# Optimization experiments

Hardware: AMD Instinct MI355X
Metric: run time of the kernel (lower is better)

Reference implementation:

```python
import jax, jax.numpy as jnp
import numpy as np
import math

B, S, HID = 2, 2048, 2048
H, HKV, D, L = 16, 4, 128, 64
THETA = 10000.0
N_REP = H // HKV


def _rope(t, pos, theta=THETA):
    # t: [B, h, S, D], pos: [B, S] int
    d = t.shape[-1]
    inv_freq = 1.0 / (theta ** (jnp.arange(0, d, 2, dtype=jnp.float32) / d))  # [d/2]
    ang = pos.astype(jnp.float32)[:, :, None] * inv_freq  # [B, S, d/2]
    cos = jnp.concatenate([jnp.cos(ang), jnp.cos(ang)], axis=-1)[:, None]  # [B,1,S,d]
    sin = jnp.concatenate([jnp.sin(ang), jnp.sin(ang)], axis=-1)[:, None]
    t1, t2 = t[..., : d // 2], t[..., d // 2 :]
    rot = jnp.concatenate([-t2, t1], axis=-1)
    return t * cos + rot * sin


def setup_inputs() -> dict:
    key = jax.random.key(0)
    ks = jax.random.split(key, 9)
    sc = lambda fin: 1.0 / math.sqrt(fin)
    x = jax.random.normal(ks[0], (B, S, HID), dtype=jnp.float32)
    position_ids = jnp.broadcast_to(jnp.arange(S, dtype=jnp.int32), (B, S))
    # additive causal mask [1,1,S,S]
    causal = jnp.triu(jnp.full((S, S), -1e9, dtype=jnp.float32), k=1)
    attention_mask = causal[None, None]
    Wq = jax.random.normal(ks[1], (HID, H * D), dtype=jnp.float32) * sc(HID)
    Wk = jax.random.normal(ks[2], (HID, HKV * D), dtype=jnp.float32) * sc(HID)
    Wv = jax.random.normal(ks[3], (HID, HKV * D), dtype=jnp.float32) * sc(HID)
    Wql = jax.random.normal(ks[4], (D, L), dtype=jnp.float32) * sc(D)
    Wkl = jax.random.normal(ks[5], (D, L), dtype=jnp.float32) * sc(D)
    Wvl = jax.random.normal(ks[6], (D, L), dtype=jnp.float32) * sc(D)
    Wo = jax.random.normal(ks[7], (H * D, HID), dtype=jnp.float32) * sc(H * D)
    return {"x": x, "position_ids": position_ids, "attention_mask": attention_mask,
            "Wq": Wq, "Wk": Wk, "Wv": Wv, "Wql": Wql, "Wkl": Wkl, "Wvl": Wvl, "Wo": Wo}


def reference(x, position_ids, attention_mask, Wq, Wk, Wv, Wql, Wkl, Wvl, Wo):
    b, s, _ = x.shape
    q = (x @ Wq).reshape(b, s, H, D).transpose(0, 2, 1, 3)    # [B,H,S,D]
    k = (x @ Wk).reshape(b, s, HKV, D).transpose(0, 2, 1, 3)  # [B,HKV,S,D]
    v = (x @ Wv).reshape(b, s, HKV, D).transpose(0, 2, 1, 3)
    q = _rope(q, position_ids)
    k = _rope(k, position_ids)
    # latent compression per head-dim
    q_l = jnp.einsum('bhsd,dl->bhsl', q, Wql)  # [B,H,S,L]
    k_l = jnp.einsum('bhsd,dl->bhsl', k, Wkl)  # [B,HKV,S,L]
    v_l = jnp.einsum('bhsd,dl->bhsl', v, Wvl)
    k_l = jnp.repeat(k_l, N_REP, axis=1)  # repeat_kv -> [B,H,S,L]
    v_l = jnp.repeat(v_l, N_REP, axis=1)
    scale = math.sqrt(L)
    attn = jnp.einsum('bhql,bhkl->bhqk', q_l, k_l) / scale
    attn = attn + attention_mask
    attn = jax.nn.softmax(attn, axis=-1)
    out = jnp.einsum('bhqk,bhkl->bhql', attn, v_l)  # [B,H,S,L]
    if L < D:
        out = jnp.pad(out, ((0, 0), (0, 0), (0, 0), (0, D - L)))
    out = out.transpose(0, 2, 1, 3).reshape(b, s, H * D)
    return out @ Wo
```

## Files before the change

### kernel.cpp

```cpp
#include <hip/hip_runtime.h>
#include <cstddef>

constexpr int kB   = 2;
constexpr int kS   = 2048;
constexpr int kHID = 2048;
constexpr int kH   = 16;
constexpr int kHKV = 4;
constexpr int kD   = 128;
constexpr int kL   = 64;
constexpr int kTok = kB * kS;
constexpr int kNQKV = kH * kD + 2 * kHKV * kD;

typedef __attribute__((ext_vector_type(8))) short bf16x8;
typedef __attribute__((ext_vector_type(4))) float f32x4;

static __device__ __forceinline__ short f2bf(float f) {
  union { float f; unsigned u; } v{f};
  const unsigned r = (v.u + 0x7fff + ((v.u >> 16) & 1)) >> 16;
  return (short)r;
}
static __device__ __forceinline__ float bf2f(short s) {
  union { unsigned u; float f; } v;
  v.u = ((unsigned)(unsigned short)s) << 16;
  return v.f;
}

static __device__ __forceinline__ bf16x8 pack8(float4 a, float4 b) {
  bf16x8 r;
  r[0] = f2bf(a.x); r[1] = f2bf(a.y); r[2] = f2bf(a.z); r[3] = f2bf(a.w);
  r[4] = f2bf(b.x); r[5] = f2bf(b.y); r[6] = f2bf(b.z); r[7] = f2bf(b.w);
  return r;
}

static __device__ __forceinline__ unsigned cvt_pk_bf16(float lo, float hi) {
  unsigned r;
  asm("v_cvt_pk_bf16_f32 %0, %1, %2" : "=v"(r) : "v"(lo), "v"(hi));
  return r;
}

typedef __attribute__((address_space(3))) void       lds_void;
typedef __attribute__((address_space(1))) const void gm_void;
static __device__ __forceinline__ void gload16(const void* g, void* l) {
  __builtin_amdgcn_global_load_lds((gm_void*)g, (lds_void*)l, 16, 0, 0);
}

static __device__ __forceinline__ int2 xcd_swz(int nx, int ny) {
  int wg = blockIdx.y * nx + blockIdx.x;
  const int cpx = (nx * ny) >> 3;
  wg = (wg & 7) * cpx + (wg >> 3);
  int2 r; r.x = wg % nx; r.y = wg / nx;
  return r;
}

__global__ __launch_bounds__(256) void cvt_bf16(const float* __restrict__ in,
                                                short* __restrict__ out, int n8) {
  const int i = blockIdx.x * 256 + threadIdx.x;
  if (i >= n8) return;
  const float4 a = *(const float4*)&in[i * 8];
  const float4 b = *(const float4*)&in[i * 8 + 4];
  *(bf16x8*)&out[i * 8] = pack8(a, b);
}

__global__ __launch_bounds__(256) void trig_table(const int* __restrict__ pos,
                                                  float* __restrict__ tbl) {
  const int idx = blockIdx.x * 256 + threadIdx.x;
  if (idx >= kTok * 64) return;
  const int i = idx & 63, t = idx >> 6;
  const float p = (float)pos[t];
  const float inv_freq = expf(-(float)i * (9.210340371976184f / 64.0f));
  const float ang = p * inv_freq;
  tbl[t * 128 + i]      = cosf(ang);
  tbl[t * 128 + 64 + i] = sinf(ang);
}

__global__ __launch_bounds__(256) void transpose_qkv(
    const float* __restrict__ Wq, const float* __restrict__ Wk,
    const float* __restrict__ Wv, short* __restrict__ out) {
  __shared__ float T[64][65];
  const int n0 = blockIdx.x * 64, k0 = blockIdx.y * 64;
  const float* in; int Nin, nl0;
  if (n0 < 2048)      { in = Wq; Nin = 2048; nl0 = n0; }
  else if (n0 < 2560) { in = Wk; Nin = 512;  nl0 = n0 - 2048; }
  else                { in = Wv; Nin = 512;  nl0 = n0 - 2560; }
  const int tid = threadIdx.x;
  const int rr = tid >> 4, cc = tid & 15;
#pragma unroll
  for (int ii = 0; ii < 4; ++ii) {
    const int kr = rr + ii * 16;
    const float4 v = *(const float4*)&in[(size_t)(k0 + kr) * Nin + nl0 + cc * 4];
    T[kr][cc * 4 + 0] = v.x; T[kr][cc * 4 + 1] = v.y;
    T[kr][cc * 4 + 2] = v.z; T[kr][cc * 4 + 3] = v.w;
  }
  __syncthreads();
#pragma unroll
  for (int ii = 0; ii < 4; ++ii) {
    const int n = rr + ii * 16;
    const short4 s4 = make_short4(f2bf(T[cc * 4 + 0][n]), f2bf(T[cc * 4 + 1][n]),
                                  f2bf(T[cc * 4 + 2][n]), f2bf(T[cc * 4 + 3][n]));
    *(short4*)&out[(size_t)(n0 + n) * kHID + k0 + cc * 4] = s4;
  }
}

template <bool REMAP>
__global__ __launch_bounds__(256) void transpose_cvt(
    const float* __restrict__ in, short* __restrict__ out,
    int Nin, int out_ld, int row_off, float scale) {
  __shared__ float T[64][65];
  const int tid = threadIdx.x;
  const int k0 = blockIdx.y * 64, n0 = blockIdx.x * 64;
  const int rr = tid >> 4;
  const int cc = tid & 15;
#pragma unroll
  for (int ii = 0; ii < 4; ++ii) {
    const int kr = rr + ii * 16;
    int gr = k0 + kr;
    if (REMAP) gr = ((gr >> 6) << 7) + (gr & 63);
    const float4 v = *(const float4*)&in[(size_t)gr * Nin + n0 + cc * 4];
    T[kr][cc * 4 + 0] = v.x * scale; T[kr][cc * 4 + 1] = v.y * scale;
    T[kr][cc * 4 + 2] = v.z * scale; T[kr][cc * 4 + 3] = v.w * scale;
  }
  __syncthreads();
#pragma unroll
  for (int ii = 0; ii < 4; ++ii) {
    const int n = rr + ii * 16;
    const short4 s4 = make_short4(f2bf(T[cc * 4 + 0][n]), f2bf(T[cc * 4 + 1][n]),
                                  f2bf(T[cc * 4 + 2][n]), f2bf(T[cc * 4 + 3][n]));
    *(short4*)&out[(size_t)(row_off + n0 + n) * out_ld + k0 + cc * 4] = s4;
  }
}

__global__ __launch_bounds__(256) void transpose_lat3(
    const float* __restrict__ Wql, const float* __restrict__ Wkl,
    const float* __restrict__ Wvl, short* __restrict__ WqlT,
    short* __restrict__ WklT, short* __restrict__ WvlT) {
  __shared__ float T[64][65];
  const float* in; short* out; float scale;
  if (blockIdx.z == 0)      { in = Wql; out = WqlT; scale = 0.125f; }
  else if (blockIdx.z == 1) { in = Wkl; out = WklT; scale = 1.0f; }
  else                      { in = Wvl; out = WvlT; scale = 1.0f; }
  const int tid = threadIdx.x;
  const int k0 = blockIdx.y * 64;
  const int rr = tid >> 4, cc = tid & 15;
#pragma unroll
  for (int ii = 0; ii < 4; ++ii) {
    const int kr = rr + ii * 16;
    const float4 v = *(const float4*)&in[(size_t)(k0 + kr) * kL + cc * 4];
    T[kr][cc * 4 + 0] = v.x * scale; T[kr][cc * 4 + 1] = v.y * scale;
    T[kr][cc * 4 + 2] = v.z * scale; T[kr][cc * 4 + 3] = v.w * scale;
  }
  __syncthreads();
#pragma unroll
  for (int ii = 0; ii < 4; ++ii) {
    const int n = rr + ii * 16;
    const short4 s4 = make_short4(f2bf(T[cc * 4 + 0][n]), f2bf(T[cc * 4 + 1][n]),
                                  f2bf(T[cc * 4 + 2][n]), f2bf(T[cc * 4 + 3][n]));
    *(short4*)&out[(size_t)n * kD + k0 + cc * 4] = s4;
  }
}

__global__ __launch_bounds__(512) void gemm_qkv8(
    const short* __restrict__ A, const short* __restrict__ Bt,
    short* __restrict__ C0, short* __restrict__ C1, short* __restrict__ C2,
    int K) {
  __shared__ short As[2][256 * 64];
  __shared__ short Bs[2][256 * 64];
  const int tid = threadIdx.x;
  const int lane = tid & 63, w = tid >> 6;
  const int lr = lane & 15, lk = lane >> 4;
  const int wm = w >> 2, wn = w & 3;
  const int2 sw = xcd_swz(kNQKV / 256, kTok / 256);
  const int row0 = sw.y * 256, col0 = sw.x * 256;
  const int NT = K >> 6;

  auto stage = [&](int kt) {
    const int b = kt & 1;
    const int k0 = kt << 6;
#pragma unroll
    for (int j = 0; j < 4; ++j) {
      const int idx = j * 512 + tid;
      const int row = idx >> 3, blk = idx & 7;
      const int gcol = k0 + ((blk ^ (row & 7)) << 3);
      gload16(A + (size_t)(row0 + row) * K + gcol, &As[b][row * 64 + blk * 8]);
    }
#pragma unroll
    for (int j = 0; j < 4; ++j) {
      const int idx = j * 512 + tid;
      const int row = idx >> 3, blk = idx & 7;
      const int gcol = k0 + ((blk ^ (row & 7)) << 3);
      gload16(Bt + (size_t)(col0 + row) * K + gcol, &Bs[b][row * 64 + blk * 8]);
    }
  };

  f32x4 acc[8][4] = {};

  stage(0);
  for (int t = 0; t < NT; ++t) {
    const int b = t & 1;
    if (t + 1 < NT) {
      stage(t + 1);
      asm volatile("s_waitcnt vmcnt(8)" ::: "memory");
    } else {
      asm volatile("s_waitcnt vmcnt(0)" ::: "memory");
    }
    __builtin_amdgcn_s_barrier();

    bf16x8 bb[4][2];
#pragma unroll
    for (int n = 0; n < 4; ++n) {
      const int row = wn * 64 + n * 16 + lr;
#pragma unroll
      for (int ch = 0; ch < 2; ++ch) {
        const int blk = (ch * 4 + lk) ^ (row & 7);
        bb[n][ch] = *(const bf16x8*)&Bs[b][row * 64 + blk * 8];
      }
    }
#pragma unroll
    for (int qm = 0; qm < 2; ++qm) {
      bf16x8 a[4][2];
#pragma unroll
      for (int j = 0; j < 4; ++j) {
        const int row = wm * 128 + (qm * 4 + j) * 16 + lr;
#pragma unroll
        for (int ch = 0; ch < 2; ++ch) {
          const int blk = (ch * 4 + lk) ^ (row & 7);
          a[j][ch] = *(const bf16x8*)&As[b][row * 64 + blk * 8];
        }
      }
      __builtin_amdgcn_s_setprio(1);
#pragma unroll
      for (int j = 0; j < 4; ++j)
#pragma unroll
        for (int n = 0; n < 4; ++n)
#pragma unroll
          for (int ch = 0; ch < 2; ++ch)
            acc[qm * 4 + j][n] = __builtin_amdgcn_mfma_f32_16x16x32_bf16(
                a[j][ch], bb[n][ch], acc[qm * 4 + j][n], 0, 0, 0);
      __builtin_amdgcn_s_setprio(0);
    }
    __builtin_amdgcn_s_barrier();
  }

  short* dst; int ld, cb;
  if (col0 < 2048)      { dst = C0; ld = 2048; cb = col0; }
  else if (col0 < 2560) { dst = C1; ld = 512;  cb = col0 - 2048; }
  else                  { dst = C2; ld = 512;  cb = col0 - 2560; }
  const int crow0 = row0 + wm * 128 + lk * 4;
  const int ccol0 = cb + wn * 64 + lr;
#pragma unroll
  for (int mf = 0; mf < 8; ++mf)
#pragma unroll
    for (int nf = 0; nf < 4; ++nf)
#pragma unroll
      for (int r = 0; r < 4; ++r)
        dst[(size_t)(crow0 + mf * 16 + r) * ld + ccol0 + nf * 16] =
            f2bf(acc[mf][nf][r]);
}

__global__ __launch_bounds__(512) void gemm_out8(
    const short* __restrict__ A, const short* __restrict__ Bt,
    float* __restrict__ C, int M, int N, int K) {
  __shared__ short As[2][256 * 64];
  __shared__ short Bs[2][128 * 64];
  const int tid = threadIdx.x;
  const int lane = tid & 63, w = tid >> 6;
  const int lr = lane & 15, lk = lane >> 4;
  const int wm = w >> 2, wn = w & 3;
  const int2 sw = xcd_swz(N / 128, M / 256);
  const int row0 = sw.y * 256, col0 = sw.x * 128;
  const int NT = K >> 6;

  auto stage = [&](int kt) {
    const int b = kt & 1;
    const int k0 = kt << 6;
#pragma unroll
    for (int j = 0; j < 4; ++j) {
      const int idx = j * 512 + tid;
      const int row = idx >> 3, blk = idx & 7;
      const int gcol = k0 + ((blk ^ (row & 7)) << 3);
      gload16(A + (size_t)(row0 + row) * K + gcol, &As[b][row * 64 + blk * 8]);
    }
#pragma unroll
    for (int j = 0; j < 2; ++j) {
      const int idx = j * 512 + tid;
      const int row = idx >> 3, blk = idx & 7;
      const int gcol = k0 + ((blk ^ (row & 7)) << 3);
      gload16(Bt + (size_t)(col0 + row) * K + gcol, &Bs[b][row * 64 + blk * 8]);
    }
  };

  f32x4 acc[8][2] = {};

  stage(0);
  for (int t = 0; t < NT; ++t) {
    const int b = t & 1;
    if (t + 1 < NT) {
      stage(t + 1);
      asm volatile("s_waitcnt vmcnt(6)" ::: "memory");
    } else {
      asm volatile("s_waitcnt vmcnt(0)" ::: "memory");
    }
    __builtin_amdgcn_s_barrier();

    bf16x8 bb[2][2];
#pragma unroll
    for (int n = 0; n < 2; ++n) {
      const int row = wn * 32 + n * 16 + lr;
#pragma unroll
      for (int ch = 0; ch < 2; ++ch) {
        const int blk = (ch * 4 + lk) ^ (row & 7);
        bb[n][ch] = *(const bf16x8*)&Bs[b][row * 64 + blk * 8];
      }
    }
#pragma unroll
    for (int qm = 0; qm < 2; ++qm) {
      bf16x8 a[4][2];
#pragma unroll
      for (int j = 0; j < 4; ++j) {
        const int row = wm * 128 + (qm * 4 + j) * 16 + lr;
#pragma unroll
        for (int ch = 0; ch < 2; ++ch) {
          const int blk = (ch * 4 + lk) ^ (row & 7);
          a[j][ch] = *(const bf16x8*)&As[b][row * 64 + blk * 8];
        }
      }
      __builtin_amdgcn_s_setprio(1);
#pragma unroll
      for (int j = 0; j < 4; ++j)
#pragma unroll
        for (int n = 0; n < 2; ++n)
#pragma unroll
          for (int ch = 0; ch < 2; ++ch)
            acc[qm * 4 + j][n] = __builtin_amdgcn_mfma_f32_16x16x32_bf16(
                a[j][ch], bb[n][ch], acc[qm * 4 + j][n], 0, 0, 0);
      __builtin_amdgcn_s_setprio(0);
    }
    __builtin_amdgcn_s_barrier();
  }

  const int crow0 = row0 + wm * 128 + lk * 4;
  const int ccol0 = col0 + wn * 32 + lr;
#pragma unroll
  for (int mf = 0; mf < 8; ++mf)
#pragma unroll
    for (int nf = 0; nf < 2; ++nf)
#pragma unroll
      for (int r = 0; r < 4; ++r)
        C[(size_t)(crow0 + mf * 16 + r) * N + ccol0 + nf * 16] = acc[mf][nf][r];
}

__global__ __launch_bounds__(256) void rope_latent_all(
    const short* __restrict__ qb, const short* __restrict__ kb,
    const short* __restrict__ vb, const short* __restrict__ WqlT,
    const short* __restrict__ WklT, const short* __restrict__ WvlT,
    const float* __restrict__ tbl, short* __restrict__ q_l,
    short* __restrict__ k_l, short* __restrict__ v_lT) {
  __shared__ short Tw[4][1280];
  const int yz = blockIdx.y;
  const short* in; const short* WT; short* out; int nh; bool ROPE, TR;
  int bh;
  if (yz < 32)      { in = qb; WT = WqlT; out = q_l;  nh = kH;   ROPE = true;  TR = false; bh = yz; }
  else if (yz < 40) { in = kb; WT = WklT; out = k_l;  nh = kHKV; ROPE = true;  TR = false; bh = yz - 32; }
  else              { in = vb; WT = WvlT; out = v_lT; nh = kHKV; ROPE = false; TR = true;  bh = yz - 40; }

  const int tid = threadIdx.x;
  const int lane = tid & 63;
  const int w = tid >> 6;
  const int lr = lane & 15;
  const int lk = lane >> 4;
  const int b = bh / nh, h = bh % nh;
  const int s0 = blockIdx.x * 64;
  const int srow = s0 + w * 16 + lr;
  const int tok = b * kS + srow;

  const short* ip = in + ((size_t)tok * nh + h) * kD + lk * 8;
  bf16x8 raw[4];
#pragma unroll
  for (int ch = 0; ch < 4; ++ch) raw[ch] = *(const bf16x8*)(ip + ch * 32);

  bf16x8 af[4];
  if (ROPE) {
    float a[4][8];
#pragma unroll
    for (int ch = 0; ch < 4; ++ch)
#pragma unroll
      for (int i = 0; i < 8; ++i) a[ch][i] = bf2f(raw[ch][i]);
    const float* tb = tbl + (size_t)tok * 128;
    float c[2][8], sn[2][8];
#pragma unroll
    for (int g = 0; g < 2; ++g) {
      const float4 cA = *(const float4*)(tb + g * 32 + lk * 8);
      const float4 cB = *(const float4*)(tb + g * 32 + lk * 8 + 4);
      const float4 sA = *(const float4*)(tb + 64 + g * 32 + lk * 8);
      const float4 sB = *(const float4*)(tb + 64 + g * 32 + lk * 8 + 4);
      c[g][0] = cA.x; c[g][1] = cA.y; c[g][2] = cA.z; c[g][3] = cA.w;
      c[g][4] = cB.x; c[g][5] = cB.y; c[g][6] = cB.z; c[g][7] = cB.w;
      sn[g][0] = sA.x; sn[g][1] = sA.y; sn[g][2] = sA.z; sn[g][3] = sA.w;
      sn[g][4] = sB.x; sn[g][5] = sB.y; sn[g][6] = sB.z; sn[g][7] = sB.w;
    }
    float o[4][8];
#pragma unroll
    for (int g = 0; g < 2; ++g)
#pragma unroll
      for (int i = 0; i < 8; ++i) {
        o[g][i]     = a[g][i]     * c[g][i] - a[g + 2][i] * sn[g][i];
        o[g + 2][i] = a[g + 2][i] * c[g][i] + a[g][i]     * sn[g][i];
      }
#pragma unroll
    for (int ch = 0; ch < 4; ++ch)
#pragma unroll
      for (int i = 0; i < 8; ++i) af[ch][i] = f2bf(o[ch][i]);
  } else {
#pragma unroll
    for (int ch = 0; ch < 4; ++ch) af[ch] = raw[ch];
  }

  f32x4 acc[4] = {};
#pragma unroll
  for (int cb = 0; cb < 4; ++cb) {
#pragma unroll
    for (int ch = 0; ch < 4; ++ch) {
      const bf16x8 bfrag =
          *(const bf16x8*)&WT[(size_t)(cb * 16 + lr) * kD + ch * 32 + lk * 8];
      acc[cb] = __builtin_amdgcn_mfma_f32_16x16x32_bf16(af[ch], bfrag,
                                                        acc[cb], 0, 0, 0);
    }
  }

  short* T = Tw[w];
  if (!TR) {
#pragma unroll
    for (int cb = 0; cb < 4; ++cb)
#pragma unroll
      for (int r = 0; r < 4; ++r)
        T[(lk * 4 + r) * 72 + cb * 16 + lr] = f2bf(acc[cb][r]);
    asm volatile("s_waitcnt lgkmcnt(0)" ::: "memory");
#pragma unroll
    for (int it = 0; it < 2; ++it) {
      const int idx = it * 64 + lane;
      const int row = idx >> 3, c8 = (idx & 7) << 3;
      *(bf16x8*)&out[((size_t)bh * kS + s0 + w * 16 + row) * kL + c8] =
          *(const bf16x8*)&T[row * 72 + c8];
    }
  } else {
#pragma unroll
    for (int cb = 0; cb < 4; ++cb)
#pragma unroll
      for (int r = 0; r < 4; ++r)
        T[(cb * 16 + lr) * 20 + lk * 4 + r] = f2bf(acc[cb][r]);
    asm volatile("s_waitcnt lgkmcnt(0)" ::: "memory");
    const size_t orow = ((size_t)bh * kL + lane) * kS + s0 + w * 16;
#pragma unroll
    for (int c = 0; c < 4; ++c)
      *(short4*)&out[orow + c * 4] = *(const short4*)&T[lane * 20 + c * 4];
  }
}

__global__ __launch_bounds__(512) void flash_attn_mfma(
    const short* __restrict__ ql, const short* __restrict__ kl,
    const short* __restrict__ vlT, short* __restrict__ attn_out) {
  constexpr int LDK = 72;
  __shared__ short Kt[2][64 * LDK];
  __shared__ short Vt[2][64 * LDK];

  const int tid = threadIdx.x;
  const int lane = tid & 63;
  const int w = tid >> 6;
  const int lr = lane & 15;
  const int lk = lane >> 4;
  const int bid = blockIdx.y;
  const int bx = (bid < 8) ? (2 * bid) : (31 - 2 * bid);
  const int q0 = bx * 128;
  const int bh = blockIdx.x;
  const int b = bh >> 4, h = bh & 15;
  const int hk = h >> 2;
  const int wrow = q0 + w * 16;

  const short* qrow = ql + ((size_t)bh * kS + wrow + lr) * kL;
  bf16x8 qf[2];
  qf[0] = *(const bf16x8*)(qrow + lk * 8);
  qf[1] = *(const bf16x8*)(qrow + 32 + lk * 8);

  f32x4 Of[4] = {};
  float m = -3.0e38f, l = 0.f;

  const size_t kbase = (size_t)(b * kHKV + hk) * kS * kL;
  const size_t vbase = (size_t)(b * kHKV + hk) * kL * kS;
  const int ntiles = q0 / 64 + 2;
  const int sr = tid >> 3, sc8 = (tid & 7) << 3;
  const short* kp = kl + kbase + (size_t)sr * kL + sc8;
  const short* vp = vlT + vbase + (size_t)sr * kS + sc8;

  *(bf16x8*)&Kt[0][sr * LDK + sc8] = *(const bf16x8*)kp;
  *(bf16x8*)&Vt[0][sr * LDK + sc8] = *(const bf16x8*)vp;
  __syncthreads();

  const int sl0 = lr + ((lane & 16) << 1);
  const bool hi = (lk >> 1) != 0;

  int cur = 0;
  for (int t = 0; t < ntiles; ++t) {
    const int j0 = t * 64;
    const bool pre = (t + 1 < ntiles);
    bf16x8 krn, vrn;
    if (pre) {
      krn = *(const bf16x8*)(kp + (size_t)(j0 + 64) * kL);
      vrn = *(const bf16x8*)(vp + (j0 + 64));
    }

    if (j0 <= wrow) {
      const short* Kc = &Kt[cur][0];
      const short* Vc = &Vt[cur][0];

      f32x4 Sf[4];
      __builtin_amdgcn_s_setprio(1);
#pragma unroll
      for (int cb = 0; cb < 4; ++cb) {
        f32x4 acc = {};
#pragma unroll
        for (int ch = 0; ch < 2; ++ch) {
          const bf16x8 kf = *(const bf16x8*)&Kc[(cb * 16 + lr) * LDK + ch * 32 + lk * 8];
          acc = __builtin_amdgcn_mfma_f32_16x16x32_bf16(kf, qf[ch], acc, 0, 0, 0);
        }
        Sf[cb] = acc;
      }
      __builtin_amdgcn_s_setprio(0);

      float mt = -3.0e38f;
      if (j0 + 63 > wrow) {
#pragma unroll
        for (int cb = 0; cb < 4; ++cb)
#pragma unroll
          for (int r = 0; r < 4; ++r) {
            float s = Sf[cb][r];
            if ((j0 + cb * 16 + lk * 4 + r) > (wrow + lr)) s = -3.0e38f;
            Sf[cb][r] = s;
            mt = fmaxf(mt, s);
          }
      } else {
#pragma unroll
        for (int cb = 0; cb < 4; ++cb)
#pragma unroll
          for (int r = 0; r < 4; ++r) mt = fmaxf(mt, Sf[cb][r]);
      }
      mt = fmaxf(mt, __shfl_xor(mt, 16));
      mt = fmaxf(mt, __shfl_xor(mt, 32));

      const bool resc = __any((int)(mt > m + 8.f));
      if (resc) {
        const float mnew = fmaxf(m, mt);
        const float corr = __expf(m - mnew);
        m = mnew;
        l *= corr;
#pragma unroll
        for (int lb = 0; lb < 4; ++lb)
#pragma unroll
          for (int r = 0; r < 4; ++r) Of[lb][r] *= corr;
      }

      unsigned pk[4][2];
#pragma unroll
      for (int cb = 0; cb < 4; ++cb) {
        const float p0 = __expf(Sf[cb][0] - m);
        const float p1 = __expf(Sf[cb][1] - m);
        const float p2 = __expf(Sf[cb][2] - m);
        const float p3 = __expf(Sf[cb][3] - m);
        l += (p0 + p1) + (p2 + p3);
        pk[cb][0] = cvt_pk_bf16(p0, p1);
        pk[cb][1] = cvt_pk_bf16(p2, p3);
      }

#pragma unroll
      for (int ch = 0; ch < 2; ++ch) {
        const unsigned lo00 = __shfl(pk[2 * ch][0], sl0);
        const unsigned lo01 = __shfl(pk[2 * ch][1], sl0);
        const unsigned lo10 = __shfl(pk[2 * ch][0], sl0 + 16);
        const unsigned lo11 = __shfl(pk[2 * ch][1], sl0 + 16);
        const unsigned hi00 = __shfl(pk[2 * ch + 1][0], sl0);
        const unsigned hi01 = __shfl(pk[2 * ch + 1][1], sl0);
        const unsigned hi10 = __shfl(pk[2 * ch + 1][0], sl0 + 16);
        const unsigned hi11 = __shfl(pk[2 * ch + 1][1], sl0 + 16);
        union { unsigned u[4]; bf16x8 v; } pf;
        pf.u[0] = hi ? hi00 : lo00;
        pf.u[1] = hi ? hi01 : lo01;
        pf.u[2] = hi ? hi10 : lo10;
        pf.u[3] = hi ? hi11 : lo11;
        __builtin_amdgcn_s_setprio(1);
#pragma unroll
        for (int lb = 0; lb < 4; ++lb) {
          const bf16x8 vf = *(const bf16x8*)&Vc[(lb * 16 + lr) * LDK + ch * 32 + lk * 8];
          Of[lb] = __builtin_amdgcn_mfma_f32_16x16x32_bf16(vf, pf.v, Of[lb], 0, 0, 0);
        }
        __builtin_amdgcn_s_setprio(0);
      }
    }

    if (pre) {
      *(bf16x8*)&Kt[cur ^ 1][sr * LDK + sc8] = krn;
      *(bf16x8*)&Vt[cur ^ 1][sr * LDK + sc8] = vrn;
    }
    __syncthreads();
    cur ^= 1;
  }

  l += __shfl_xor(l, 16);
  l += __shfl_xor(l, 32);
  const float inv = 1.f / l;
  const size_t rowoff =
      (size_t)(b * kS + wrow + lr) * (kH * kL) + h * kL + lk * 4;
#pragma unroll
  for (int lb = 0; lb < 4; ++lb) {
    const short4 s4 = make_short4(f2bf(Of[lb][0] * inv), f2bf(Of[lb][1] * inv),
                                  f2bf(Of[lb][2] * inv), f2bf(Of[lb][3] * inv));
    *(short4*)&attn_out[rowoff + lb * 16] = s4;
  }
}

extern "C" void kernel_launch(void* const* d_in, const int* in_sizes, int n_in,
                              void* d_out, int out_size, void* d_ws, size_t ws_size,
                              hipStream_t stream) {
  const float* x    = (const float*)d_in[0];
  const int*   pos  = (const int*)d_in[1];
  const float* Wq   = (const float*)d_in[3];
  const float* Wk   = (const float*)d_in[4];
  const float* Wv   = (const float*)d_in[5];
  const float* Wql  = (const float*)d_in[6];
  const float* Wkl  = (const float*)d_in[7];
  const float* Wvl  = (const float*)d_in[8];
  const float* Wo   = (const float*)d_in[9];
  float* out = (float*)d_out;

  char* p = (char*)d_ws;
  short* x_bf  = (short*)p; p += (size_t)kTok * kHID * 2;
  short* Wqkv  = (short*)p; p += (size_t)kNQKV * kHID * 2;
  short* WoT   = (short*)p; p += (size_t)kHID * (kH * kL) * 2;
  short* WqlT  = (short*)p; p += (size_t)kL * kD * 2;
  short* WklT  = (short*)p; p += (size_t)kL * kD * 2;
  short* WvlT  = (short*)p; p += (size_t)kL * kD * 2;
  float* tbl   = (float*)p; p += (size_t)kTok * 128 * 4;
  short* k_buf = (short*)p; p += (size_t)kTok * kHKV * kD * 2;
  short* v_buf = (short*)p; p += (size_t)kTok * kHKV * kD * 2;
  short* q_l   = (short*)p; p += (size_t)kB * kH * kS * kL * 2;
  short* k_l   = (short*)p; p += (size_t)kB * kHKV * kS * kL * 2;
  short* v_lT  = (short*)p; p += (size_t)kB * kHKV * kS * kL * 2;
  short* attn  = (short*)p;
  short* q_buf = (short*)d_out;

  cvt_bf16<<<kTok * kHID / 8 / 256, 256, 0, stream>>>(x, x_bf, kTok * kHID / 8);
  trig_table<<<kTok * 64 / 256, 256, 0, stream>>>(pos, tbl);
  transpose_qkv<<<dim3(kNQKV / 64, kHID / 64), 256, 0, stream>>>(
      Wq, Wk, Wv, Wqkv);
  transpose_cvt<true><<<dim3(kHID / 64, (kH * kL) / 64), 256, 0, stream>>>(
      Wo, WoT, kHID, kH * kL, 0, 1.0f);
  transpose_lat3<<<dim3(1, kD / 64, 3), 256, 0, stream>>>(
      Wql, Wkl, Wvl, WqlT, WklT, WvlT);

  gemm_qkv8<<<dim3(kNQKV / 256, kTok / 256), 512, 0, stream>>>(
      x_bf, Wqkv, q_buf, k_buf, v_buf, kHID);

  rope_latent_all<<<dim3(kS / 64, 48), 256, 0, stream>>>(
      q_buf, k_buf, v_buf, WqlT, WklT, WvlT, tbl, q_l, k_l, v_lT);

  flash_attn_mfma<<<dim3(kB * kH, kS / 128), 512, 0, stream>>>(
      q_l, k_l, v_lT, attn);

  gemm_out8<<<dim3(kHID / 128, kTok / 256), 512, 0, stream>>>(
      attn, WoT, out, kTok, kHID, kH * kL);
}
```

Baseline: 194.1 us.

## Merge prep kernels into one launch and widen flash-attention KV tiles to 128

```diff
diff --git a/kernel.cpp b/kernel.cpp
--- a/kernel.cpp
+++ b/kernel.cpp
@@ -52,109 +52,105 @@
   return r;
 }
 
-__global__ __launch_bounds__(256) void cvt_bf16(const float* __restrict__ in,
-                                                short* __restrict__ out, int n8) {
-  const int i = blockIdx.x * 256 + threadIdx.x;
-  if (i >= n8) return;
-  const float4 a = *(const float4*)&in[i * 8];
-  const float4 b = *(const float4*)&in[i * 8 + 4];
-  *(bf16x8*)&out[i * 8] = pack8(a, b);
-}
-
-__global__ __launch_bounds__(256) void trig_table(const int* __restrict__ pos,
-                                                  float* __restrict__ tbl) {
-  const int idx = blockIdx.x * 256 + threadIdx.x;
-  if (idx >= kTok * 64) return;
-  const int i = idx & 63, t = idx >> 6;
-  const float p = (float)pos[t];
-  const float inv_freq = expf(-(float)i * (9.210340371976184f / 64.0f));
-  const float ang = p * inv_freq;
-  tbl[t * 128 + i]      = cosf(ang);
-  tbl[t * 128 + 64 + i] = sinf(ang);
-}
-
-__global__ __launch_bounds__(256) void transpose_qkv(
+__global__ __launch_bounds__(256) void prep_all(
+    const float* __restrict__ x, const int* __restrict__ pos,
     const float* __restrict__ Wq, const float* __restrict__ Wk,
-    const float* __restrict__ Wv, short* __restrict__ out) {
-  __shared__ float T[64][65];
-  const int n0 = blockIdx.x * 64, k0 = blockIdx.y * 64;
-  const float* in; int Nin, nl0;
-  if (n0 < 2048)      { in = Wq; Nin = 2048; nl0 = n0; }
-  else if (n0 < 2560) { in = Wk; Nin = 512;  nl0 = n0 - 2048; }
-  else                { in = Wv; Nin = 512;  nl0 = n0 - 2560; }
-  const int tid = threadIdx.x;
-  const int rr = tid >> 4, cc = tid & 15;
-#pragma unroll
-  for (int ii = 0; ii < 4; ++ii) {
-    const int kr = rr + ii * 16;
-    const float4 v = *(const float4*)&in[(size_t)(k0 + kr) * Nin + nl0 + cc * 4];
-    T[kr][cc * 4 + 0] = v.x; T[kr][cc * 4 + 1] = v.y;
-    T[kr][cc * 4 + 2] = v.z; T[kr][cc * 4 + 3] = v.w;
-  }
-  __syncthreads();
-#pragma unroll
-  for (int ii = 0; ii < 4; ++ii) {
-    const int n = rr + ii * 16;
-    const short4 s4 = make_short4(f2bf(T[cc * 4 + 0][n]), f2bf(T[cc * 4 + 1][n]),
-                                  f2bf(T[cc * 4 + 2][n]), f2bf(T[cc * 4 + 3][n]));
-    *(short4*)&out[(size_t)(n0 + n) * kHID + k0 + cc * 4] = s4;
-  }
-}
-
-template <bool REMAP>
-__global__ __launch_bounds__(256) void transpose_cvt(
-    const float* __restrict__ in, short* __restrict__ out,
-    int Nin, int out_ld, int row_off, float scale) {
-  __shared__ float T[64][65];
-  const int tid = threadIdx.x;
-  const int k0 = blockIdx.y * 64, n0 = blockIdx.x * 64;
-  const int rr = tid >> 4;
-  const int cc = tid & 15;
-#pragma unroll
-  for (int ii = 0; ii < 4; ++ii) {
-    const int kr = rr + ii * 16;
-    int gr = k0 + kr;
-    if (REMAP) gr = ((gr >> 6) << 7) + (gr & 63);
-    const float4 v = *(const float4*)&in[(size_t)gr * Nin + n0 + cc * 4];
-    T[kr][cc * 4 + 0] = v.x * scale; T[kr][cc * 4 + 1] = v.y * scale;
-    T[kr][cc * 4 + 2] = v.z * scale; T[kr][cc * 4 + 3] = v.w * scale;
-  }
-  __syncthreads();
-#pragma unroll
-  for (int ii = 0; ii < 4; ++ii) {
-    const int n = rr + ii * 16;
-    const short4 s4 = make_short4(f2bf(T[cc * 4 + 0][n]), f2bf(T[cc * 4 + 1][n]),
-                                  f2bf(T[cc * 4 + 2][n]), f2bf(T[cc * 4 + 3][n]));
-    *(short4*)&out[(size_t)(row_off + n0 + n) * out_ld + k0 + cc * 4] = s4;
-  }
-}
-
-__global__ __launch_bounds__(256) void transpose_lat3(
+    const float* __restrict__ Wv, const float* __restrict__ Wo,
     const float* __restrict__ Wql, const float* __restrict__ Wkl,
-    const float* __restrict__ Wvl, short* __restrict__ WqlT,
+    const float* __restrict__ Wvl, short* __restrict__ x_bf,
+    float* __restrict__ tbl, short* __restrict__ Wqkv,
+    short* __restrict__ WoT, short* __restrict__ WqlT,
     short* __restrict__ WklT, short* __restrict__ WvlT) {
   __shared__ float T[64][65];
-  const float* in; short* out; float scale;
-  if (blockIdx.z == 0)      { in = Wql; out = WqlT; scale = 0.125f; }
-  else if (blockIdx.z == 1) { in = Wkl; out = WklT; scale = 1.0f; }
-  else                      { in = Wvl; out = WvlT; scale = 1.0f; }
+  const int bidg = blockIdx.x;
   const int tid = threadIdx.x;
-  const int k0 = blockIdx.y * 64;
+
+  if (bidg < 4096) {
+    const int i = bidg * 256 + tid;
+    const float4 a = *(const float4*)&x[(size_t)i * 8];
+    const float4 b = *(const float4*)&x[(size_t)i * 8 + 4];
+    *(bf16x8*)&x_bf[(size_t)i * 8] = pack8(a, b);
+    return;
+  }
+  if (bidg < 5120) {
+    const int idx = (bidg - 4096) * 256 + tid;
+    const int i = idx & 63, t = idx >> 6;
+    const float p = (float)pos[t];
+    const float inv_freq = expf(-(float)i * (9.210340371976184f / 64.0f));
+    const float ang = p * inv_freq;
+    tbl[t * 128 + i]      = cosf(ang);
+    tbl[t * 128 + 64 + i] = sinf(ang);
+    return;
+  }
   const int rr = tid >> 4, cc = tid & 15;
-#pragma unroll
-  for (int ii = 0; ii < 4; ++ii) {
-    const int kr = rr + ii * 16;
-    const float4 v = *(const float4*)&in[(size_t)(k0 + kr) * kL + cc * 4];
-    T[kr][cc * 4 + 0] = v.x * scale; T[kr][cc * 4 + 1] = v.y * scale;
-    T[kr][cc * 4 + 2] = v.z * scale; T[kr][cc * 4 + 3] = v.w * scale;
-  }
-  __syncthreads();
-#pragma unroll
-  for (int ii = 0; ii < 4; ++ii) {
-    const int n = rr + ii * 16;
-    const short4 s4 = make_short4(f2bf(T[cc * 4 + 0][n]), f2bf(T[cc * 4 + 1][n]),
-                                  f2bf(T[cc * 4 + 2][n]), f2bf(T[cc * 4 + 3][n]));
-    *(short4*)&out[(size_t)n * kD + k0 + cc * 4] = s4;
+  if (bidg < 6656) {
+    const int idx = bidg - 5120;
+    const int n0 = (idx % 48) * 64, k0 = (idx / 48) * 64;
+    const float* in; int Nin, nl0;
+    if (n0 < 2048)      { in = Wq; Nin = 2048; nl0 = n0; }
+    else if (n0 < 2560) { in = Wk; Nin = 512;  nl0 = n0 - 2048; }
+    else                { in = Wv; Nin = 512;  nl0 = n0 - 2560; }
+#pragma unroll
+    for (int ii = 0; ii < 4; ++ii) {
+      const int kr = rr + ii * 16;
+      const float4 v = *(const float4*)&in[(size_t)(k0 + kr) * Nin + nl0 + cc * 4];
+      T[kr][cc * 4 + 0] = v.x; T[kr][cc * 4 + 1] = v.y;
+      T[kr][cc * 4 + 2] = v.z; T[kr][cc * 4 + 3] = v.w;
+    }
+    __syncthreads();
+#pragma unroll
+    for (int ii = 0; ii < 4; ++ii) {
+      const int n = rr + ii * 16;
+      const short4 s4 = make_short4(f2bf(T[cc*4+0][n]), f2bf(T[cc*4+1][n]),
+                                    f2bf(T[cc*4+2][n]), f2bf(T[cc*4+3][n]));
+      *(short4*)&Wqkv[(size_t)(n0 + n) * kHID + k0 + cc * 4] = s4;
+    }
+    return;
+  }
+  if (bidg < 7168) {
+    const int idx = bidg - 6656;
+    const int n0 = (idx % 32) * 64, k0 = (idx / 32) * 64;
+#pragma unroll
+    for (int ii = 0; ii < 4; ++ii) {
+      const int kr = rr + ii * 16;
+      const int gr = (((k0 + kr) >> 6) << 7) + ((k0 + kr) & 63);
+      const float4 v = *(const float4*)&Wo[(size_t)gr * kHID + n0 + cc * 4];
+      T[kr][cc * 4 + 0] = v.x; T[kr][cc * 4 + 1] = v.y;
+      T[kr][cc * 4 + 2] = v.z; T[kr][cc * 4 + 3] = v.w;
+    }
+    __syncthreads();
+#pragma unroll
+    for (int ii = 0; ii < 4; ++ii) {
+      const int n = rr + ii * 16;
+      const short4 s4 = make_short4(f2bf(T[cc*4+0][n]), f2bf(T[cc*4+1][n]),
+                                    f2bf(T[cc*4+2][n]), f2bf(T[cc*4+3][n]));
+      *(short4*)&WoT[(size_t)(n0 + n) * (kH * kL) + k0 + cc * 4] = s4;
+    }
+    return;
+  }
+  {
+    const int idx = bidg - 7168;
+    const int k0 = (idx & 1) * 64;
+    const int z = idx >> 1;
+    const float* in; short* out; float scale;
+    if (z == 0)      { in = Wql; out = WqlT; scale = 0.125f; }
+    else if (z == 1) { in = Wkl; out = WklT; scale = 1.0f; }
+    else             { in = Wvl; out = WvlT; scale = 1.0f; }
+#pragma unroll
+    for (int ii = 0; ii < 4; ++ii) {
+      const int kr = rr + ii * 16;
+      const float4 v = *(const float4*)&in[(size_t)(k0 + kr) * kL + cc * 4];
+      T[kr][cc * 4 + 0] = v.x * scale; T[kr][cc * 4 + 1] = v.y * scale;
+      T[kr][cc * 4 + 2] = v.z * scale; T[kr][cc * 4 + 3] = v.w * scale;
+    }
+    __syncthreads();
+#pragma unroll
+    for (int ii = 0; ii < 4; ++ii) {
+      const int n = rr + ii * 16;
+      const short4 s4 = make_short4(f2bf(T[cc*4+0][n]), f2bf(T[cc*4+1][n]),
+                                    f2bf(T[cc*4+2][n]), f2bf(T[cc*4+3][n]));
+      *(short4*)&out[(size_t)n * kD + k0 + cc * 4] = s4;
+    }
   }
 }
 
@@ -459,8 +455,9 @@
     const short* __restrict__ ql, const short* __restrict__ kl,
     const short* __restrict__ vlT, short* __restrict__ attn_out) {
   constexpr int LDK = 72;
-  __shared__ short Kt[2][64 * LDK];
-  __shared__ short Vt[2][64 * LDK];
+  constexpr int LDV = 136;
+  __shared__ short Kt[2][128 * LDK];
+  __shared__ short Vt[2][64 * LDV];
 
   const int tid = threadIdx.x;
   const int lane = tid & 63;
@@ -483,33 +480,43 @@
   f32x4 Of[4] = {};
   float m = -3.0e38f, l = 0.f;
 
-  const size_t kbase = (size_t)(b * kHKV + hk) * kS * kL;
-  const size_t vbase = (size_t)(b * kHKV + hk) * kL * kS;
-  const int ntiles = q0 / 64 + 2;
-  const int sr = tid >> 3, sc8 = (tid & 7) << 3;
-  const short* kp = kl + kbase + (size_t)sr * kL + sc8;
-  const short* vp = vlT + vbase + (size_t)sr * kS + sc8;
-
-  *(bf16x8*)&Kt[0][sr * LDK + sc8] = *(const bf16x8*)kp;
-  *(bf16x8*)&Vt[0][sr * LDK + sc8] = *(const bf16x8*)vp;
+  const short* kgp = kl + (size_t)(b * kHKV + hk) * kS * kL;
+  const short* vgp = vlT + (size_t)(b * kHKV + hk) * kL * kS;
+  const int ntiles = bx + 1;
+
+  const int kr0 = tid >> 3,          kc0 = (tid & 7) << 3;
+  const int kr1 = (512 + tid) >> 3,  kc1 = (tid & 7) << 3;
+  const int vr0 = tid >> 4,          vc0 = (tid & 15) << 3;
+  const int vr1 = (512 + tid) >> 4,  vc1 = (tid & 15) << 3;
+
+  *(bf16x8*)&Kt[0][kr0 * LDK + kc0] = *(const bf16x8*)(kgp + (size_t)kr0 * kL + kc0);
+  *(bf16x8*)&Kt[0][kr1 * LDK + kc1] = *(const bf16x8*)(kgp + (size_t)kr1 * kL + kc1);
+  *(bf16x8*)&Vt[0][vr0 * LDV + vc0] = *(const bf16x8*)(vgp + (size_t)vr0 * kS + vc0);
+  *(bf16x8*)&Vt[0][vr1 * LDV + vc1] = *(const bf16x8*)(vgp + (size_t)vr1 * kS + vc1);
   __syncthreads();
 
   const int sl0 = lr + ((lane & 16) << 1);
-  const bool hi = (lk >> 1) != 0;
+  const bool hisel = (lk >> 1) != 0;
 
   int cur = 0;
   for (int t = 0; t < ntiles; ++t) {
-    const int j0 = t * 64;
+    const int j0 = t * 128;
     const bool pre = (t + 1 < ntiles);
-    bf16x8 krn, vrn;
+    bf16x8 krn0, krn1, vrn0, vrn1;
     if (pre) {
-      krn = *(const bf16x8*)(kp + (size_t)(j0 + 64) * kL);
-      vrn = *(const bf16x8*)(vp + (j0 + 64));
-    }
-
-    if (j0 <= wrow) {
-      const short* Kc = &Kt[cur][0];
-      const short* Vc = &Vt[cur][0];
+      const int jn = j0 + 128;
+      krn0 = *(const bf16x8*)(kgp + (size_t)(jn + kr0) * kL + kc0);
+      krn1 = *(const bf16x8*)(kgp + (size_t)(jn + kr1) * kL + kc1);
+      vrn0 = *(const bf16x8*)(vgp + (size_t)vr0 * kS + jn + vc0);
+      vrn1 = *(const bf16x8*)(vgp + (size_t)vr1 * kS + jn + vc1);
+    }
+
+    const short* Kc = &Kt[cur][0];
+    const short* Vc = &Vt[cur][0];
+#pragma unroll
+    for (int sub = 0; sub < 2; ++sub) {
+      const int js = j0 + sub * 64;
+      if (js > wrow) continue;
 
       f32x4 Sf[4];
       __builtin_amdgcn_s_setprio(1);
@@ -518,7 +525,8 @@
         f32x4 acc = {};
 #pragma unroll
         for (int ch = 0; ch < 2; ++ch) {
-          const bf16x8 kf = *(const bf16x8*)&Kc[(cb * 16 + lr) * LDK + ch * 32 + lk * 8];
+          const bf16x8 kf = *(const bf16x8*)
+              &Kc[(sub * 64 + cb * 16 + lr) * LDK + ch * 32 + lk * 8];
           acc = __builtin_amdgcn_mfma_f32_16x16x32_bf16(kf, qf[ch], acc, 0, 0, 0);
         }
         Sf[cb] = acc;
@@ -526,13 +534,13 @@
       __builtin_amdgcn_s_setprio(0);
 
       float mt = -3.0e38f;
-      if (j0 + 63 > wrow) {
+      if (js + 63 > wrow) {
 #pragma unroll
         for (int cb = 0; cb < 4; ++cb)
 #pragma unroll
           for (int r = 0; r < 4; ++r) {
             float s = Sf[cb][r];
-            if ((j0 + cb * 16 + lk * 4 + r) > (wrow + lr)) s = -3.0e38f;
+            if ((js + cb * 16 + lk * 4 + r) > (wrow + lr)) s = -3.0e38f;
             Sf[cb][r] = s;
             mt = fmaxf(mt, s);
           }
@@ -580,14 +588,15 @@
         const unsigned hi10 = __shfl(pk[2 * ch + 1][0], sl0 + 16);
         const unsigned hi11 = __shfl(pk[2 * ch + 1][1], sl0 + 16);
         union { unsigned u[4]; bf16x8 v; } pf;
-        pf.u[0] = hi ? hi00 : lo00;
-        pf.u[1] = hi ? hi01 : lo01;
-        pf.u[2] = hi ? hi10 : lo10;
-        pf.u[3] = hi ? hi11 : lo11;
+        pf.u[0] = hisel ? hi00 : lo00;
+        pf.u[1] = hisel ? hi01 : lo01;
+        pf.u[2] = hisel ? hi10 : lo10;
+        pf.u[3] = hisel ? hi11 : lo11;
         __builtin_amdgcn_s_setprio(1);
 #pragma unroll
         for (int lb = 0; lb < 4; ++lb) {
-          const bf16x8 vf = *(const bf16x8*)&Vc[(lb * 16 + lr) * LDK + ch * 32 + lk * 8];
+          const bf16x8 vf = *(const bf16x8*)
+              &Vc[(lb * 16 + lr) * LDV + sub * 64 + ch * 32 + lk * 8];
           Of[lb] = __builtin_amdgcn_mfma_f32_16x16x32_bf16(vf, pf.v, Of[lb], 0, 0, 0);
         }
         __builtin_amdgcn_s_setprio(0);
@@ -595,8 +604,10 @@
     }
 
     if (pre) {
-      *(bf16x8*)&Kt[cur ^ 1][sr * LDK + sc8] = krn;
-      *(bf16x8*)&Vt[cur ^ 1][sr * LDK + sc8] = vrn;
+      *(bf16x8*)&Kt[cur ^ 1][kr0 * LDK + kc0] = krn0;
+      *(bf16x8*)&Kt[cur ^ 1][kr1 * LDK + kc1] = krn1;
+      *(bf16x8*)&Vt[cur ^ 1][vr0 * LDV + vc0] = vrn0;
+      *(bf16x8*)&Vt[cur ^ 1][vr1 * LDV + vc1] = vrn1;
     }
     __syncthreads();
     cur ^= 1;
@@ -645,14 +656,8 @@
   short* attn  = (short*)p;
   short* q_buf = (short*)d_out;
 
-  cvt_bf16<<<kTok * kHID / 8 / 256, 256, 0, stream>>>(x, x_bf, kTok * kHID / 8);
-  trig_table<<<kTok * 64 / 256, 256, 0, stream>>>(pos, tbl);
-  transpose_qkv<<<dim3(kNQKV / 64, kHID / 64), 256, 0, stream>>>(
-      Wq, Wk, Wv, Wqkv);
-  transpose_cvt<true><<<dim3(kHID / 64, (kH * kL) / 64), 256, 0, stream>>>(
-      Wo, WoT, kHID, kH * kL, 0, 1.0f);
-  transpose_lat3<<<dim3(1, kD / 64, 3), 256, 0, stream>>>(
-      Wql, Wkl, Wvl, WqlT, WklT, WvlT);
+  prep_all<<<7174, 256, 0, stream>>>(x, pos, Wq, Wk, Wv, Wo, Wql, Wkl, Wvl,
+                                     x_bf, tbl, Wqkv, WoT, WqlT, WklT, WvlT);
 
   gemm_qkv8<<<dim3(kNQKV / 256, kTok / 256), 512, 0, stream>>>(
       x_bf, Wqkv, q_buf, k_buf, v_buf, kHID);
```

Result: faster. 180.5 us, median of 2 (-7.0%).
